# Kernel tuning notes

Hardware: AMD Instinct MI355X
Metric: run time of the kernel (lower is better)

The kernel has to match this reference:

```python
import jax, jax.numpy as jnp
import numpy as np

DICE_TH = 0.4
CLS_TH = 0.5
LN_EPS = 1e-5


def setup_inputs() -> dict:
    key = jax.random.key(0)
    P, C, NC, K = 200_000, 256, 200, 24  # points, clicks, classes, latent prototypes
    ks = jax.random.split(key, 6)
    # structured masks: each click targets one of K prototype regions so the
    # dice/cls thresholds yield a non-degenerate grouping
    point_proto = jax.random.randint(ks[0], (P,), 0, K)
    proto_vals = jax.random.uniform(ks[1], (P,))
    click_proto = jax.random.randint(ks[2], (C,), 0, K)
    base = (point_proto[:, None] == click_proto[None, :]).astype(jnp.float32)  # [P, C]
    noise = jax.random.uniform(ks[3], (P, C))
    masks_heatmap = base * (0.6 + 0.4 * proto_vals[:, None]) + 0.02 * noise
    class_emb = jax.random.normal(ks[4], (K, NC)) * 3.0
    cls_logits = class_emb[click_proto] + 0.3 * jax.random.normal(ks[5], (C, NC))
    clicks_list = jax.random.randint(ks[0], (C,), 0, NC)  # unused (random_clicks=True)
    return {"masks_heatmap": masks_heatmap, "cls_logits": cls_logits,
            "clicks_list": clicks_list}


def _associate(masks_heatmap, cls_logits):
    """Greedy dice+cls-similarity grouping (random_clicks=True path).
    Returns labels[c] = leader click index of the group containing click c."""
    M = masks_heatmap                      # [P, C]
    C = M.shape[1]
    s = M.sum(0)                           # [C]
    # dice[i, j] = 2 * m_i . m_j / (sum(m_i) + sum(m_j))  (all pairs at once)
    dice = 2.0 * (M.T @ M) / (s[:, None] + s[None, :])
    # F.layer_norm over last dim, no affine
    mu = cls_logits.mean(-1, keepdims=True)
    var = ((cls_logits - mu) ** 2).mean(-1, keepdims=True)
    p = (cls_logits - mu) / jnp.sqrt(var + LN_EPS)
    sim = p @ p.T                          # [C, C]
    cond = (dice > DICE_TH) & (sim > CLS_TH)

    def step(carry, x):
        assigned, labels = carry
        i, row = x
        # skip if i already suppressed; take unsuppressed clicks matching row i
        take = row & (~assigned) & (~assigned[i])
        return (assigned | take, jnp.where(take, i, labels)), None

    init = (jnp.zeros((C,), bool), jnp.full((C,), -1, jnp.int32))
    (assigned, labels), _ = jax.lax.scan(
        step, init, (jnp.arange(C, dtype=jnp.int32), cond))
    return labels


def _merge(labels, masks_heatmap, cls_logits):
    """reduction='max': per-group max over member clicks. Unused group slots
    (non-leader indices) are zero-filled and flagged by group_valid."""
    C = masks_heatmap.shape[1]
    seg = jnp.where(labels >= 0, labels, C)  # route unassigned to dump segment
    counts = jax.ops.segment_sum(jnp.ones((C,), jnp.float32), seg,
                                 num_segments=C + 1)[:C]
    group_valid = counts > 0
    nm = jax.ops.segment_max(masks_heatmap.T, seg, num_segments=C + 1)[:C]  # [C, P]
    nc = jax.ops.segment_max(cls_logits, seg, num_segments=C + 1)[:C]      # [C, NC]
    new_masks = jnp.where(group_valid[:, None], nm, 0.0).T  # [P, C]
    new_cls = jnp.where(group_valid[:, None], nc, 0.0)      # [C, NC]
    return new_masks, new_cls, group_valid


def reference(masks_heatmap, cls_logits, clicks_list):
    labels = _associate(masks_heatmap, cls_logits)
    new_masks, new_cls, group_valid = _merge(labels, masks_heatmap, cls_logits)
    return labels, group_valid, new_masks, new_cls
```

## Files before the change

### kernel.cpp

```cpp
#include <hip/hip_runtime.h>
#include <cstdint>
#include <cstddef>

constexpr int P  = 200000;
constexpr int C  = 256;
constexpr int NC = 200;
#define DICE_TH 0.4f
#define CLS_TH  0.5f
#define LN_EPS  1e-5f

constexpr int KC = 1600;
constexpr int NCHUNK = 125;
constexpr int NSTEP = KC / 32;

constexpr size_t WS_G       = 0;
constexpr size_t WS_S       = 262144;
constexpr size_t WS_PROW    = 263168;
constexpr size_t WS_PT      = 467968;
constexpr size_t WS_COND    = 672768;
constexpr size_t WS_MSTART  = 680960;
constexpr size_t WS_MEMBERS = 682240;
constexpr size_t WS_PART    = 1048576;
constexpr size_t PART_BYTES = (size_t)NCHUNK * 3 * 16384 * 4;

typedef float floatx4 __attribute__((ext_vector_type(4)));
typedef float floatx16 __attribute__((ext_vector_type(16)));
typedef __bf16 bf16x4 __attribute__((ext_vector_type(4)));
typedef __bf16 bf16x8 __attribute__((ext_vector_type(8)));
typedef unsigned short ushort4v __attribute__((ext_vector_type(4)));
typedef unsigned short ushort8 __attribute__((ext_vector_type(8)));

constexpr int LDA = 40;

__global__ __launch_bounds__(256, 2) void gram_mfma_kernel(
    const float* __restrict__ M, float* __restrict__ G, float* __restrict__ s,
    float* __restrict__ part) {
  __shared__ unsigned short Abf[128 * LDA];
  __shared__ unsigned short Bbf[128 * LDA];
  __shared__ float scol[128];

  const int type = blockIdx.x;
  const int i0 = (type == 2) ? 128 : 0;
  const int j0 = (type == 0) ? 0 : 128;
  const bool diag = (type != 1);
  const int tid = threadIdx.x;
  const int wv = tid >> 6, lane = tid & 63;
  const int wr = wv >> 1, wc = wv & 1;
  const int g  = tid & 31;
  const int kq = tid >> 5;
  const int chunk = blockIdx.y;
  const int k0 = chunk * KC;

  if (tid < 128) scol[tid] = 0.f;

  floatx16 acc[4];
#pragma unroll
  for (int t = 0; t < 4; ++t)
#pragma unroll
    for (int r = 0; r < 16; ++r) acc[t][r] = 0.f;
  float ss[4] = {0.f, 0.f, 0.f, 0.f};

  const int mrow = lane & 31;
  const int kgrp = (lane >> 5) * 8;
  const int xa = ((mrow >> 2) & 3) << 1;
  const int wbase = (kq ^ ((g & 3) << 1)) << 2;

  const float* baseA = M + i0 + 4 * g;
  const float* baseB = M + j0 + 4 * g;

#define LOADS(dst, base, step_)                                              \
  {                                                                          \
    const float* src_ = (base) + (size_t)(k0 + (step_) * 32 + 4 * kq) * 256; \
    dst[0] = *reinterpret_cast<const floatx4*>(src_);                        \
    dst[1] = *reinterpret_cast<const floatx4*>(src_ + 256);                  \
    dst[2] = *reinterpret_cast<const floatx4*>(src_ + 512);                  \
    dst[3] = *reinterpret_cast<const floatx4*>(src_ + 768);                  \
  }

#define STAGE(dstLds, r_)                                                    \
  {                                                                          \
    _Pragma("unroll") for (int cc = 0; cc < 4; ++cc) {                       \
      floatx4 f = {r_[0][cc], r_[1][cc], r_[2][cc], r_[3][cc]};              \
      bf16x4 b = __builtin_convertvector(f, bf16x4);                         \
      *reinterpret_cast<ushort4v*>(&dstLds[(4 * g + cc) * LDA + wbase]) =    \
          __builtin_bit_cast(ushort4v, b);                                   \
    }                                                                        \
  }

#define SSUM(r_)                                                             \
  if (diag) {                                                                \
    ss[0] += r_[0][0] + r_[1][0] + r_[2][0] + r_[3][0];                      \
    ss[1] += r_[0][1] + r_[1][1] + r_[2][1] + r_[3][1];                      \
    ss[2] += r_[0][2] + r_[1][2] + r_[2][2] + r_[3][2];                      \
    ss[3] += r_[0][3] + r_[1][3] + r_[2][3] + r_[3][3];                      \
  }

#define MFMA_STEP()                                                          \
  {                                                                          \
    const unsigned short* Bsrc = diag ? Abf : Bbf;                           \
    _Pragma("unroll") for (int sub = 0; sub < 2; ++sub) {                    \
      const int ko = sub * 16 + kgrp;                                        \
      const int koff = (((ko >> 2) ^ xa) << 2);                              \
      bf16x8 av0 = __builtin_bit_cast(                                       \
          bf16x8, *reinterpret_cast<const ushort8*>(                         \
                      &Abf[(64 * wr + mrow) * LDA + koff]));                 \
      bf16x8 av1 = __builtin_bit_cast(                                       \
          bf16x8, *reinterpret_cast<const ushort8*>(                         \
                      &Abf[(64 * wr + 32 + mrow) * LDA + koff]));            \
      bf16x8 bv0 = __builtin_bit_cast(                                       \
          bf16x8, *reinterpret_cast<const ushort8*>(                         \
                      &Bsrc[(64 * wc + mrow) * LDA + koff]));                \
      bf16x8 bv1 = __builtin_bit_cast(                                       \
          bf16x8, *reinterpret_cast<const ushort8*>(                         \
                      &Bsrc[(64 * wc + 32 + mrow) * LDA + koff]));           \
      acc[0] = __builtin_amdgcn_mfma_f32_32x32x16_bf16(av0, bv0, acc[0], 0, 0, 0); \
      acc[1] = __builtin_amdgcn_mfma_f32_32x32x16_bf16(av0, bv1, acc[1], 0, 0, 0); \
      acc[2] = __builtin_amdgcn_mfma_f32_32x32x16_bf16(av1, bv0, acc[2], 0, 0, 0); \
      acc[3] = __builtin_amdgcn_mfma_f32_32x32x16_bf16(av1, bv1, acc[3], 0, 0, 0); \
    }                                                                        \
  }

  floatx4 a0[4], a1[4], b0[4], b1[4];
  LOADS(a0, baseA, 0);
  if (!diag) LOADS(b0, baseB, 0);

  for (int sp = 0; sp < NSTEP; sp += 2) {
    SSUM(a0);
    STAGE(Abf, a0);
    if (!diag) STAGE(Bbf, b0);
    __syncthreads();
    LOADS(a1, baseA, sp + 1);
    if (!diag) LOADS(b1, baseB, sp + 1);
    MFMA_STEP();
    __syncthreads();

    SSUM(a1);
    STAGE(Abf, a1);
    if (!diag) STAGE(Bbf, b1);
    __syncthreads();
    if (sp + 2 < NSTEP) {
      LOADS(a0, baseA, sp + 2);
      if (!diag) LOADS(b0, baseB, sp + 2);
    }
    MFMA_STEP();
    __syncthreads();
  }
#undef LOADS
#undef STAGE
#undef SSUM
#undef MFMA_STEP

  if (part != nullptr) {
    float* Pp = part + ((size_t)chunk * 3 + type) * 16384;
#pragma unroll
    for (int ai = 0; ai < 2; ++ai)
#pragma unroll
      for (int bj = 0; bj < 2; ++bj)
#pragma unroll
        for (int r = 0; r < 16; ++r) {
          const int lr = 64 * wr + 32 * ai + (r & 3) + 8 * (r >> 2) + 4 * (lane >> 5);
          const int lc = 64 * wc + 32 * bj + (lane & 31);
          Pp[lr * 128 + lc] = acc[ai * 2 + bj][r];
        }
  } else {
#pragma unroll
    for (int ai = 0; ai < 2; ++ai)
#pragma unroll
      for (int bj = 0; bj < 2; ++bj)
#pragma unroll
        for (int r = 0; r < 16; ++r) {
          const int gr = i0 + 64 * wr + 32 * ai + (r & 3) + 8 * (r >> 2) + 4 * (lane >> 5);
          const int gc = j0 + 64 * wc + 32 * bj + (lane & 31);
          atomicAdd(&G[(size_t)gr * 256 + gc], acc[ai * 2 + bj][r]);
        }
  }
  if (diag) {
#pragma unroll
    for (int cc = 0; cc < 4; ++cc) atomicAdd(&scol[4 * g + cc], ss[cc]);
    __syncthreads();
    if (tid < 128) atomicAdd(&s[i0 + tid], scol[tid]);
  }
}

__global__ __launch_bounds__(128) void reduce_g_kernel(
    const float* __restrict__ part, float* __restrict__ G) {
  const int slot = blockIdx.x >> 7;
  const int lr = blockIdx.x & 127;
  const int lc = threadIdx.x;
  const float* src = part + (size_t)slot * 16384 + (size_t)lr * 128 + lc;
  float s0 = 0.f, s1 = 0.f, s2 = 0.f, s3 = 0.f, s4 = 0.f;
  int ch = 0;
  for (; ch + 5 <= NCHUNK; ch += 5) {
    s0 += src[(size_t)(ch + 0) * 49152];
    s1 += src[(size_t)(ch + 1) * 49152];
    s2 += src[(size_t)(ch + 2) * 49152];
    s3 += src[(size_t)(ch + 3) * 49152];
    s4 += src[(size_t)(ch + 4) * 49152];
  }
  for (; ch < NCHUNK; ++ch) s0 += src[(size_t)ch * 49152];
  const int i0 = (slot == 2) ? 128 : 0;
  const int j0 = (slot == 0) ? 0 : 128;
  G[(size_t)(i0 + lr) * 256 + (j0 + lc)] = ((s0 + s1) + (s2 + s3)) + s4;
}

__global__ __launch_bounds__(64) void ln_kernel(const float* __restrict__ cls,
                                                float* __restrict__ p_row,
                                                float* __restrict__ pT) {
  const int c = blockIdx.x;
  const int t = threadIdx.x;
  const float* x = cls + (size_t)c * NC;
  float v0 = x[t];
  float v1 = x[t + 64];
  float v2 = (t < 72) ? x[t + 128] : 0.f;

  float sum = v0 + v1 + v2;
#pragma unroll
  for (int o = 32; o > 0; o >>= 1) sum += __shfl_xor(sum, o);
  const float mu = sum / (float)NC;

  float d0 = v0 - mu, d1 = v1 - mu, d2 = (t < 72) ? (v2 - mu) : 0.f;
  float sq = d0 * d0 + d1 * d1 + d2 * d2;
#pragma unroll
  for (int o = 32; o > 0; o >>= 1) sq += __shfl_xor(sq, o);
  const float var = sq / (float)NC;
  const float inv = 1.0f / sqrtf(var + LN_EPS);

  float p0 = d0 * inv, p1 = d1 * inv, p2 = d2 * inv;
  p_row[(size_t)c * NC + t] = p0;
  p_row[(size_t)c * NC + t + 64] = p1;
  pT[(size_t)t * C + c] = p0;
  pT[(size_t)(t + 64) * C + c] = p1;
  if (t < 72) {
    p_row[(size_t)c * NC + t + 128] = p2;
    pT[(size_t)(t + 128) * C + c] = p2;
  }
}

__global__ __launch_bounds__(256) void cond_kernel(
    const float* __restrict__ G, const float* __restrict__ s,
    const float* __restrict__ p_row, const float* __restrict__ pT,
    unsigned long long* __restrict__ condW) {
  __shared__ float pi[NC];
  const int i = blockIdx.x;
  const int j = threadIdx.x;
  if (j < NC) pi[j] = p_row[(size_t)i * NC + j];
  __syncthreads();

  const float si = s[i];
  const float sj = s[j];
  const float g = (i >= 128 && j < 128) ? G[(size_t)j * C + i]
                                        : G[(size_t)i * C + j];
  const float dice = 2.f * g / (si + sj);

  float acc = 0.f;
#pragma unroll 8
  for (int k = 0; k < NC; ++k) acc = fmaf(pi[k], pT[(size_t)k * C + j], acc);

  const bool cnd = (dice > DICE_TH) && (acc > CLS_TH);
  unsigned long long m = __ballot(cnd);
  if ((j & 63) == 0) condW[i * 4 + (j >> 6)] = m;
}

__global__ __launch_bounds__(64) void scan_kernel(
    const unsigned long long* __restrict__ condW,
    float* __restrict__ out_labels, float* __restrict__ out_valid,
    int* __restrict__ mstart, int* __restrict__ members) {
  __shared__ unsigned long long cS[C * 4];
  __shared__ int cnt[C];
  __shared__ int ms[C + 1];
  const int t = threadIdx.x;

  for (int idx = t; idx < C * 4; idx += 64) cS[idx] = condW[idx];
  for (int idx = t; idx < C; idx += 64) cnt[idx] = 0;
  __syncthreads();

  unsigned long long asg[4] = {0ull, 0ull, 0ull, 0ull};
  int lab[4] = {-1, -1, -1, -1};

#pragma unroll
  for (int w = 0; w < 4; ++w) {
    for (int b = 0; b < 64; ++b) {
      const int i = w * 64 + b;
      if (!((asg[w] >> b) & 1ull)) {
#pragma unroll
        for (int w2 = 0; w2 < 4; ++w2) {
          unsigned long long tk = cS[i * 4 + w2] & ~asg[w2];
          asg[w2] |= tk;
          if ((tk >> t) & 1ull) lab[w2] = i;
        }
      }
    }
  }

#pragma unroll
  for (int w = 0; w < 4; ++w)
    if (lab[w] >= 0) atomicAdd(&cnt[lab[w]], 1);
  __syncthreads();

  if (t == 0) {
    ms[0] = 0;
    for (int c2 = 0; c2 < C; ++c2) ms[c2 + 1] = ms[c2] + cnt[c2];
  }
  __syncthreads();
  for (int idx = t; idx < C; idx += 64) cnt[idx] = ms[idx];
  __syncthreads();
#pragma unroll
  for (int w = 0; w < 4; ++w) {
    if (lab[w] >= 0) {
      int pos = atomicAdd(&cnt[lab[w]], 1);
      members[pos] = w * 64 + t;
    }
  }
#pragma unroll
  for (int w = 0; w < 4; ++w) {
    const int col = w * 64 + t;
    out_labels[col] = (float)lab[w];
    out_valid[col] = (ms[col + 1] > ms[col]) ? 1.0f : 0.0f;
  }
  for (int idx = t; idx < C + 1; idx += 64) mstart[idx] = ms[idx];
}

__global__ __launch_bounds__(256) void merge_masks_kernel(
    const float* __restrict__ M, const int* __restrict__ mstart,
    const int* __restrict__ members, float* __restrict__ out_masks) {
  __shared__ float rows[8 * 256];
  __shared__ int msS[C + 1];
  __shared__ int memS[C];
  const int tid = threadIdx.x;
  const size_t p0 = (size_t)blockIdx.x * 8;

  msS[tid] = mstart[tid];
  if (tid == 0) msS[C] = mstart[C];
  memS[tid] = members[tid];

  const float4* src = reinterpret_cast<const float4*>(M + p0 * 256);
#pragma unroll
  for (int it = 0; it < 2; ++it)
    reinterpret_cast<float4*>(rows)[it * 256 + tid] = src[it * 256 + tid];
  __syncthreads();

  const int st = msS[tid], en = msS[tid + 1];
  float mx[8];
  if (en > st) {
    const int m0 = memS[st];
#pragma unroll
    for (int r = 0; r < 8; ++r) mx[r] = rows[r * 256 + m0];
    for (int k = st + 1; k < en; ++k) {
      const int mm = memS[k];
#pragma unroll
      for (int r = 0; r < 8; ++r) mx[r] = fmaxf(mx[r], rows[r * 256 + mm]);
    }
  } else {
#pragma unroll
    for (int r = 0; r < 8; ++r) mx[r] = 0.f;
  }
  __syncthreads();
#pragma unroll
  for (int r = 0; r < 8; ++r) rows[r * 256 + tid] = mx[r];
  __syncthreads();

  const int r2 = tid >> 6;
  const int cg = (tid & 63) << 2;
#pragma unroll
  for (int pass = 0; pass < 2; ++pass) {
    const int rr = pass * 4 + r2;
    floatx4 v = *reinterpret_cast<const floatx4*>(&rows[rr * 256 + cg]);
    __builtin_nontemporal_store(
        v, reinterpret_cast<floatx4*>(&out_masks[(p0 + rr) * 256 + cg]));
  }
}

__global__ __launch_bounds__(256) void merge_cls_kernel(
    const float* __restrict__ cls, const int* __restrict__ mstart,
    const int* __restrict__ members, float* __restrict__ out_cls) {
  __shared__ int se[2];
  const int c = blockIdx.x;
  const int t = threadIdx.x;
  if (t < 2) se[t] = mstart[c + t];
  __syncthreads();
  const int st = se[0], en = se[1];
  if (t < NC) {
    float mx = 0.f;
    if (en > st) {
      mx = cls[(size_t)members[st] * NC + t];
      for (int k = st + 1; k < en; ++k)
        mx = fmaxf(mx, cls[(size_t)members[k] * NC + t]);
    }
    out_cls[(size_t)c * NC + t] = mx;
  }
}

extern "C" void kernel_launch(void* const* d_in, const int* in_sizes, int n_in,
                              void* d_out, int out_size, void* d_ws,
                              size_t ws_size, hipStream_t stream) {
  const float* M = (const float*)d_in[0];
  const float* cls = (const float*)d_in[1];

  float* out = (float*)d_out;
  char* ws = (char*)d_ws;
  float* G = (float*)(ws + WS_G);
  float* s = (float*)(ws + WS_S);
  float* p_row = (float*)(ws + WS_PROW);
  float* pT = (float*)(ws + WS_PT);
  unsigned long long* condW = (unsigned long long*)(ws + WS_COND);
  int* mstart = (int*)(ws + WS_MSTART);
  int* members = (int*)(ws + WS_MEMBERS);

  float* out_labels = out;
  float* out_valid = out + 256;
  float* out_masks = out + 512;
  float* out_cls = out + 512 + (size_t)P * 256;

  const bool bigws = ws_size >= WS_PART + PART_BYTES;
  float* part = bigws ? (float*)(ws + WS_PART) : nullptr;

  if (bigws) {
    hipMemsetAsync(ws + WS_S, 0, 1024, stream);
  } else {
    hipMemsetAsync(ws, 0, WS_S + 1024, stream);
  }

  gram_mfma_kernel<<<dim3(3, NCHUNK), 256, 0, stream>>>(M, G, s, part);
  if (bigws) reduce_g_kernel<<<384, 128, 0, stream>>>(part, G);
  ln_kernel<<<C, 64, 0, stream>>>(cls, p_row, pT);
  cond_kernel<<<C, 256, 0, stream>>>(G, s, p_row, pT, condW);
  scan_kernel<<<1, 64, 0, stream>>>(condW, out_labels, out_valid, mstart,
                                    members);
  merge_masks_kernel<<<P / 8, 256, 0, stream>>>(M, mstart, members, out_masks);
  merge_cls_kernel<<<C, 256, 0, stream>>>(cls, mstart, members, out_cls);
}
```

Baseline: 417.6 us.

## Compute full 256x256 Gram per K-chunk block and fuse partial reduction into cond

The Gram kernel now has each 512-thread block compute the full 256x256 tile for its K-chunk, so M is loaded once per chunk instead of three times (two diagonal blocks plus one off-diagonal). The K-chunk size is halved to keep enough blocks, and the lower triangle is now computed redundantly. The separate reduce kernel is removed and the partial-sum reduction over chunks moves into cond_kernel. The merge kernel processes 16 rows per block instead of 8. The partial buffer grows in size and cond_kernel now reads more memory.

```diff
diff --git a/kernel.cpp b/kernel.cpp
--- a/kernel.cpp
+++ b/kernel.cpp
@@ -9,8 +9,8 @@
 #define CLS_TH  0.5f
 #define LN_EPS  1e-5f
 
-constexpr int KC = 1600;
-constexpr int NCHUNK = 125;
+constexpr int KC = 800;
+constexpr int NCHUNK = 250;
 constexpr int NSTEP = KC / 32;
 
 constexpr size_t WS_G       = 0;
@@ -21,7 +21,7 @@
 constexpr size_t WS_MSTART  = 680960;
 constexpr size_t WS_MEMBERS = 682240;
 constexpr size_t WS_PART    = 1048576;
-constexpr size_t PART_BYTES = (size_t)NCHUNK * 3 * 16384 * 4;
+constexpr size_t PART_BYTES = (size_t)NCHUNK * 65536 * 4;
 
 typedef float floatx4 __attribute__((ext_vector_type(4)));
 typedef float floatx16 __attribute__((ext_vector_type(16)));
@@ -32,30 +32,25 @@
 
 constexpr int LDA = 40;
 
-__global__ __launch_bounds__(256, 2) void gram_mfma_kernel(
+__global__ __launch_bounds__(512, 2) void gram_mfma_kernel(
     const float* __restrict__ M, float* __restrict__ G, float* __restrict__ s,
     float* __restrict__ part) {
-  __shared__ unsigned short Abf[128 * LDA];
-  __shared__ unsigned short Bbf[128 * LDA];
-  __shared__ float scol[128];
-
-  const int type = blockIdx.x;
-  const int i0 = (type == 2) ? 128 : 0;
-  const int j0 = (type == 0) ? 0 : 128;
-  const bool diag = (type != 1);
+  __shared__ unsigned short Abf[256 * LDA];
+  __shared__ float scol[256];
+
   const int tid = threadIdx.x;
   const int wv = tid >> 6, lane = tid & 63;
   const int wr = wv >> 1, wc = wv & 1;
-  const int g  = tid & 31;
-  const int kq = tid >> 5;
-  const int chunk = blockIdx.y;
+  const int g  = tid & 63;
+  const int kq = tid >> 6;
+  const int chunk = blockIdx.x;
   const int k0 = chunk * KC;
 
-  if (tid < 128) scol[tid] = 0.f;
-
-  floatx16 acc[4];
-#pragma unroll
-  for (int t = 0; t < 4; ++t)
+  if (tid < 256) scol[tid] = 0.f;
+
+  floatx16 acc[8];
+#pragma unroll
+  for (int t = 0; t < 8; ++t)
 #pragma unroll
     for (int r = 0; r < 16; ++r) acc[t][r] = 0.f;
   float ss[4] = {0.f, 0.f, 0.f, 0.f};
@@ -65,39 +60,33 @@
   const int xa = ((mrow >> 2) & 3) << 1;
   const int wbase = (kq ^ ((g & 3) << 1)) << 2;
 
-  const float* baseA = M + i0 + 4 * g;
-  const float* baseB = M + j0 + 4 * g;
-
-#define LOADS(dst, base, step_)                                              \
+  const float* baseA = M + 4 * g;
+
+#define LOADS(dst, step_)                                                    \
   {                                                                          \
-    const float* src_ = (base) + (size_t)(k0 + (step_) * 32 + 4 * kq) * 256; \
+    const float* src_ = baseA + (size_t)(k0 + (step_) * 32 + 4 * kq) * 256;  \
     dst[0] = *reinterpret_cast<const floatx4*>(src_);                        \
     dst[1] = *reinterpret_cast<const floatx4*>(src_ + 256);                  \
     dst[2] = *reinterpret_cast<const floatx4*>(src_ + 512);                  \
     dst[3] = *reinterpret_cast<const floatx4*>(src_ + 768);                  \
   }
 
-#define STAGE(dstLds, r_)                                                    \
+#define STAGE(r_)                                                            \
   {                                                                          \
-    _Pragma("unroll") for (int cc = 0; cc < 4; ++cc) {                       \
-      floatx4 f = {r_[0][cc], r_[1][cc], r_[2][cc], r_[3][cc]};              \
-      bf16x4 b = __builtin_convertvector(f, bf16x4);                         \
-      *reinterpret_cast<ushort4v*>(&dstLds[(4 * g + cc) * LDA + wbase]) =    \
-          __builtin_bit_cast(ushort4v, b);                                   \
-    }                                                                        \
-  }
-
-#define SSUM(r_)                                                             \
-  if (diag) {                                                                \
     ss[0] += r_[0][0] + r_[1][0] + r_[2][0] + r_[3][0];                      \
     ss[1] += r_[0][1] + r_[1][1] + r_[2][1] + r_[3][1];                      \
     ss[2] += r_[0][2] + r_[1][2] + r_[2][2] + r_[3][2];                      \
     ss[3] += r_[0][3] + r_[1][3] + r_[2][3] + r_[3][3];                      \
+    _Pragma("unroll") for (int cc = 0; cc < 4; ++cc) {                       \
+      floatx4 f = {r_[0][cc], r_[1][cc], r_[2][cc], r_[3][cc]};              \
+      bf16x4 b = __builtin_convertvector(f, bf16x4);                         \
+      *reinterpret_cast<ushort4v*>(&Abf[(4 * g + cc) * LDA + wbase]) =       \
+          __builtin_bit_cast(ushort4v, b);                                   \
+    }                                                                        \
   }
 
 #define MFMA_STEP()                                                          \
   {                                                                          \
-    const unsigned short* Bsrc = diag ? Abf : Bbf;                           \
     _Pragma("unroll") for (int sub = 0; sub < 2; ++sub) {                    \
       const int ko = sub * 16 + kgrp;                                        \
       const int koff = (((ko >> 2) ^ xa) << 2);                              \
@@ -107,100 +96,68 @@
       bf16x8 av1 = __builtin_bit_cast(                                       \
           bf16x8, *reinterpret_cast<const ushort8*>(                         \
                       &Abf[(64 * wr + 32 + mrow) * LDA + koff]));            \
-      bf16x8 bv0 = __builtin_bit_cast(                                       \
-          bf16x8, *reinterpret_cast<const ushort8*>(                         \
-                      &Bsrc[(64 * wc + mrow) * LDA + koff]));                \
-      bf16x8 bv1 = __builtin_bit_cast(                                       \
-          bf16x8, *reinterpret_cast<const ushort8*>(                         \
-                      &Bsrc[(64 * wc + 32 + mrow) * LDA + koff]));           \
-      acc[0] = __builtin_amdgcn_mfma_f32_32x32x16_bf16(av0, bv0, acc[0], 0, 0, 0); \
-      acc[1] = __builtin_amdgcn_mfma_f32_32x32x16_bf16(av0, bv1, acc[1], 0, 0, 0); \
-      acc[2] = __builtin_amdgcn_mfma_f32_32x32x16_bf16(av1, bv0, acc[2], 0, 0, 0); \
-      acc[3] = __builtin_amdgcn_mfma_f32_32x32x16_bf16(av1, bv1, acc[3], 0, 0, 0); \
+      _Pragma("unroll") for (int bj = 0; bj < 4; ++bj) {                     \
+        bf16x8 bv = __builtin_bit_cast(                                      \
+            bf16x8, *reinterpret_cast<const ushort8*>(                       \
+                        &Abf[(128 * wc + 32 * bj + mrow) * LDA + koff]));    \
+        acc[bj] = __builtin_amdgcn_mfma_f32_32x32x16_bf16(av0, bv, acc[bj], 0, 0, 0); \
+        acc[4 + bj] = __builtin_amdgcn_mfma_f32_32x32x16_bf16(av1, bv, acc[4 + bj], 0, 0, 0); \
+      }                                                                      \
     }                                                                        \
   }
 
-  floatx4 a0[4], a1[4], b0[4], b1[4];
-  LOADS(a0, baseA, 0);
-  if (!diag) LOADS(b0, baseB, 0);
-
-  for (int sp = 0; sp < NSTEP; sp += 2) {
-    SSUM(a0);
-    STAGE(Abf, a0);
-    if (!diag) STAGE(Bbf, b0);
+  floatx4 a0[4], a1[4];
+  LOADS(a0, 0);
+
+  for (int sp = 0; sp < NSTEP - 1; sp += 2) {
+    STAGE(a0);
     __syncthreads();
-    LOADS(a1, baseA, sp + 1);
-    if (!diag) LOADS(b1, baseB, sp + 1);
+    LOADS(a1, sp + 1);
     MFMA_STEP();
     __syncthreads();
 
-    SSUM(a1);
-    STAGE(Abf, a1);
-    if (!diag) STAGE(Bbf, b1);
+    STAGE(a1);
     __syncthreads();
-    if (sp + 2 < NSTEP) {
-      LOADS(a0, baseA, sp + 2);
-      if (!diag) LOADS(b0, baseB, sp + 2);
-    }
+    LOADS(a0, sp + 2);
     MFMA_STEP();
     __syncthreads();
   }
+  STAGE(a0);
+  __syncthreads();
+  MFMA_STEP();
+  __syncthreads();
 #undef LOADS
 #undef STAGE
-#undef SSUM
 #undef MFMA_STEP
 
   if (part != nullptr) {
-    float* Pp = part + ((size_t)chunk * 3 + type) * 16384;
+    float* Pp = part + (size_t)chunk * 65536;
 #pragma unroll
     for (int ai = 0; ai < 2; ++ai)
 #pragma unroll
-      for (int bj = 0; bj < 2; ++bj)
+      for (int bj = 0; bj < 4; ++bj)
 #pragma unroll
         for (int r = 0; r < 16; ++r) {
           const int lr = 64 * wr + 32 * ai + (r & 3) + 8 * (r >> 2) + 4 * (lane >> 5);
-          const int lc = 64 * wc + 32 * bj + (lane & 31);
-          Pp[lr * 128 + lc] = acc[ai * 2 + bj][r];
+          const int lc = 128 * wc + 32 * bj + (lane & 31);
+          Pp[lr * 256 + lc] = acc[ai * 4 + bj][r];
         }
   } else {
 #pragma unroll
     for (int ai = 0; ai < 2; ++ai)
 #pragma unroll
-      for (int bj = 0; bj < 2; ++bj)
+      for (int bj = 0; bj < 4; ++bj)
 #pragma unroll
         for (int r = 0; r < 16; ++r) {
-          const int gr = i0 + 64 * wr + 32 * ai + (r & 3) + 8 * (r >> 2) + 4 * (lane >> 5);
-          const int gc = j0 + 64 * wc + 32 * bj + (lane & 31);
-          atomicAdd(&G[(size_t)gr * 256 + gc], acc[ai * 2 + bj][r]);
+          const int gr = 64 * wr + 32 * ai + (r & 3) + 8 * (r >> 2) + 4 * (lane >> 5);
+          const int gc = 128 * wc + 32 * bj + (lane & 31);
+          atomicAdd(&G[(size_t)gr * 256 + gc], acc[ai * 4 + bj][r]);
         }
   }
-  if (diag) {
-#pragma unroll
-    for (int cc = 0; cc < 4; ++cc) atomicAdd(&scol[4 * g + cc], ss[cc]);
-    __syncthreads();
-    if (tid < 128) atomicAdd(&s[i0 + tid], scol[tid]);
-  }
-}
-
-__global__ __launch_bounds__(128) void reduce_g_kernel(
-    const float* __restrict__ part, float* __restrict__ G) {
-  const int slot = blockIdx.x >> 7;
-  const int lr = blockIdx.x & 127;
-  const int lc = threadIdx.x;
-  const float* src = part + (size_t)slot * 16384 + (size_t)lr * 128 + lc;
-  float s0 = 0.f, s1 = 0.f, s2 = 0.f, s3 = 0.f, s4 = 0.f;
-  int ch = 0;
-  for (; ch + 5 <= NCHUNK; ch += 5) {
-    s0 += src[(size_t)(ch + 0) * 49152];
-    s1 += src[(size_t)(ch + 1) * 49152];
-    s2 += src[(size_t)(ch + 2) * 49152];
-    s3 += src[(size_t)(ch + 3) * 49152];
-    s4 += src[(size_t)(ch + 4) * 49152];
-  }
-  for (; ch < NCHUNK; ++ch) s0 += src[(size_t)ch * 49152];
-  const int i0 = (slot == 2) ? 128 : 0;
-  const int j0 = (slot == 0) ? 0 : 128;
-  G[(size_t)(i0 + lr) * 256 + (j0 + lc)] = ((s0 + s1) + (s2 + s3)) + s4;
+#pragma unroll
+  for (int cc = 0; cc < 4; ++cc) atomicAdd(&scol[4 * g + cc], ss[cc]);
+  __syncthreads();
+  if (tid < 256) atomicAdd(&s[tid], scol[tid]);
 }
 
 __global__ __launch_bounds__(64) void ln_kernel(const float* __restrict__ cls,
@@ -237,20 +194,35 @@
 }
 
 __global__ __launch_bounds__(256) void cond_kernel(
-    const float* __restrict__ G, const float* __restrict__ s,
-    const float* __restrict__ p_row, const float* __restrict__ pT,
-    unsigned long long* __restrict__ condW) {
+    const float* __restrict__ G, const float* __restrict__ part,
+    const float* __restrict__ s, const float* __restrict__ p_row,
+    const float* __restrict__ pT, unsigned long long* __restrict__ condW) {
   __shared__ float pi[NC];
   const int i = blockIdx.x;
   const int j = threadIdx.x;
   if (j < NC) pi[j] = p_row[(size_t)i * NC + j];
   __syncthreads();
 
+  float gsum;
+  if (part != nullptr) {
+    const float* src = part + (size_t)i * 256 + j;
+    float s0 = 0.f, s1 = 0.f, s2 = 0.f, s3 = 0.f, s4 = 0.f;
+#pragma unroll 1
+    for (int ch = 0; ch < NCHUNK; ch += 5) {
+      s0 += src[(size_t)(ch + 0) * 65536];
+      s1 += src[(size_t)(ch + 1) * 65536];
+      s2 += src[(size_t)(ch + 2) * 65536];
+      s3 += src[(size_t)(ch + 3) * 65536];
+      s4 += src[(size_t)(ch + 4) * 65536];
+    }
+    gsum = ((s0 + s1) + (s2 + s3)) + s4;
+  } else {
+    gsum = G[(size_t)i * C + j];
+  }
+
   const float si = s[i];
   const float sj = s[j];
-  const float g = (i >= 128 && j < 128) ? G[(size_t)j * C + i]
-                                        : G[(size_t)i * C + j];
-  const float dice = 2.f * g / (si + sj);
+  const float dice = 2.f * gsum / (si + sj);
 
   float acc = 0.f;
 #pragma unroll 8
@@ -320,14 +292,16 @@
   for (int idx = t; idx < C + 1; idx += 64) mstart[idx] = ms[idx];
 }
 
+constexpr int MROWS = 16;
+
 __global__ __launch_bounds__(256) void merge_masks_kernel(
     const float* __restrict__ M, const int* __restrict__ mstart,
     const int* __restrict__ members, float* __restrict__ out_masks) {
-  __shared__ float rows[8 * 256];
+  __shared__ float rows[MROWS * 256];
   __shared__ int msS[C + 1];
   __shared__ int memS[C];
   const int tid = threadIdx.x;
-  const size_t p0 = (size_t)blockIdx.x * 8;
+  const size_t p0 = (size_t)blockIdx.x * MROWS;
 
   msS[tid] = mstart[tid];
   if (tid == 0) msS[C] = mstart[C];
@@ -335,34 +309,34 @@
 
   const float4* src = reinterpret_cast<const float4*>(M + p0 * 256);
 #pragma unroll
-  for (int it = 0; it < 2; ++it)
+  for (int it = 0; it < MROWS / 4; ++it)
     reinterpret_cast<float4*>(rows)[it * 256 + tid] = src[it * 256 + tid];
   __syncthreads();
 
   const int st = msS[tid], en = msS[tid + 1];
-  float mx[8];
+  float mx[MROWS];
   if (en > st) {
     const int m0 = memS[st];
 #pragma unroll
-    for (int r = 0; r < 8; ++r) mx[r] = rows[r * 256 + m0];
+    for (int r = 0; r < MROWS; ++r) mx[r] = rows[r * 256 + m0];
     for (int k = st + 1; k < en; ++k) {
       const int mm = memS[k];
 #pragma unroll
-      for (int r = 0; r < 8; ++r) mx[r] = fmaxf(mx[r], rows[r * 256 + mm]);
+      for (int r = 0; r < MROWS; ++r) mx[r] = fmaxf(mx[r], rows[r * 256 + mm]);
     }
   } else {
 #pragma unroll
-    for (int r = 0; r < 8; ++r) mx[r] = 0.f;
-  }
-  __syncthreads();
-#pragma unroll
-  for (int r = 0; r < 8; ++r) rows[r * 256 + tid] = mx[r];
+    for (int r = 0; r < MROWS; ++r) mx[r] = 0.f;
+  }
+  __syncthreads();
+#pragma unroll
+  for (int r = 0; r < MROWS; ++r) rows[r * 256 + tid] = mx[r];
   __syncthreads();
 
   const int r2 = tid >> 6;
   const int cg = (tid & 63) << 2;
 #pragma unroll
-  for (int pass = 0; pass < 2; ++pass) {
+  for (int pass = 0; pass < MROWS / 4; ++pass) {
     const int rr = pass * 4 + r2;
     floatx4 v = *reinterpret_cast<const floatx4*>(&rows[rr * 256 + cg]);
     __builtin_nontemporal_store(
@@ -420,12 +394,12 @@
     hipMemsetAsync(ws, 0, WS_S + 1024, stream);
   }
 
-  gram_mfma_kernel<<<dim3(3, NCHUNK), 256, 0, stream>>>(M, G, s, part);
-  if (bigws) reduce_g_kernel<<<384, 128, 0, stream>>>(part, G);
+  gram_mfma_kernel<<<NCHUNK, 512, 0, stream>>>(M, G, s, part);
   ln_kernel<<<C, 64, 0, stream>>>(cls, p_row, pT);
-  cond_kernel<<<C, 256, 0, stream>>>(G, s, p_row, pT, condW);
+  cond_kernel<<<C, 256, 0, stream>>>(G, part, s, p_row, pT, condW);
   scan_kernel<<<1, 64, 0, stream>>>(condW, out_labels, out_valid, mstart,
                                     members);
-  merge_masks_kernel<<<P / 8, 256, 0, stream>>>(M, mstart, members, out_masks);
+  merge_masks_kernel<<<P / MROWS, 256, 0, stream>>>(M, mstart, members,
+                                                    out_masks);
   merge_cls_kernel<<<C, 256, 0, stream>>>(cls, mstart, members, out_cls);
 }
```

Result: slower. 436.3 us (+4.5%).
